# Kernel optimization log

Measured on AMD Instinct MI355X. Metric: run time of the kernel, lower is better.

The kernel has to match this reference:

```python
import jax, jax.numpy as jnp
import numpy as np

B, S, E, HD = 8, 2048, 1024, 64  # batch, seq, n_embds, head_size (n_embds // n_heads)


def setup_inputs() -> dict:
    key = jax.random.key(0)
    k1, k2, k3, k4 = jax.random.split(key, 4)
    x = jax.random.normal(k1, (B, S, E), dtype=jnp.float32)
    # torch Linear weights have shape [out_features, in_features]; scale like default init
    Wk = jax.random.normal(k2, (HD, E), dtype=jnp.float32) * (1.0 / np.sqrt(E))
    Wq = jax.random.normal(k3, (HD, E), dtype=jnp.float32) * (1.0 / np.sqrt(E))
    Wv = jax.random.normal(k4, (HD, E), dtype=jnp.float32) * (1.0 / np.sqrt(E))
    return {"x": x, "Wk": Wk, "Wq": Wq, "Wv": Wv}


def reference(x, Wk, Wq, Wv):
    # q, k, v: [B, S, HD]
    k = jnp.einsum('bse,he->bsh', x, Wk)
    q = jnp.einsum('bse,he->bsh', x, Wq)
    v = jnp.einsum('bse,he->bsh', x, Wv)
    # scores: [B, S, S], scaled by sqrt(head_size)
    scores = jnp.einsum('bqh,bkh->bqk', q, k) / jnp.sqrt(jnp.float32(HD))
    # causal mask (tril): position q attends to k <= q
    causal = jnp.tril(jnp.ones((S, S), dtype=bool))
    scores = jnp.where(causal, scores, jnp.float32(-jnp.inf))
    attn = jax.nn.softmax(scores, axis=-1)
    # dropout_rate = 0.0 -> identity
    out = jnp.einsum('bqk,bkh->bqh', attn, v)  # [B, S, HD]
    return out
```

## Files before the change

### kernel.cpp

```cpp
#include <hip/hip_runtime.h>
#include <hip/hip_bf16.h>
#include <stdint.h>

typedef short bh8 __attribute__((ext_vector_type(8)));
typedef short bh4 __attribute__((ext_vector_type(4)));
typedef float fx4 __attribute__((ext_vector_type(4)));

#define B_ 8
#define S_ 2048
#define E_ 1024
#define HD_ 64

__device__ __forceinline__ short f2bf(float f) {
  unsigned u = __builtin_bit_cast(unsigned, f);
  u = u + 0x7FFFu + ((u >> 16) & 1u);
  return (short)(u >> 16);
}

#define GL2LDS16(gp, lp) __builtin_amdgcn_global_load_lds( \
    (const __attribute__((address_space(1))) unsigned int*)(gp), \
    (__attribute__((address_space(3))) unsigned int*)(lp), 16, 0, 0)


__global__ __launch_bounds__(256) void castw_k(
    const float* __restrict__ wk, const float* __restrict__ wq,
    const float* __restrict__ wv, short* __restrict__ wc) {
  int i = blockIdx.x * 256 + threadIdx.x;
  int wsel = i >> 13;
  int o = (i & 8191) * 8;
  const float* src = (wsel == 0) ? wk : (wsel == 1) ? wq : wv;
  float4 a = *(const float4*)(src + o);
  float4 b = *(const float4*)(src + o + 4);
  bh8 r = { f2bf(a.x), f2bf(a.y), f2bf(a.z), f2bf(a.w),
            f2bf(b.x), f2bf(b.y), f2bf(b.z), f2bf(b.w) };
  *(bh8*)(wc + wsel * (HD_ * E_) + o) = r;
}

__global__ __launch_bounds__(256) void qkv_gemm(
    const float* __restrict__ x, const short* __restrict__ wc,
    short* __restrict__ kfr, short* __restrict__ qfr, short* __restrict__ vfr) {
  __shared__ short As[32 * 32];
  __shared__ short Bs[192 * 32];
  const int tid = threadIdx.x;
  const int w = tid >> 6, l = tid & 63;
  const int c = l & 15, g = l >> 4;
  const int r0 = blockIdx.x * 32;
  const int srow = l >> 2;
  const int scol = (l & 3) * 8;
  const int ar = tid >> 3;
  const int ac = (tid & 7) * 4;

  fx4 acc[2][3];
#pragma unroll
  for (int rt = 0; rt < 2; ++rt)
#pragma unroll
    for (int cc = 0; cc < 3; ++cc) acc[rt][cc] = (fx4){0.f, 0.f, 0.f, 0.f};

  for (int k0 = 0; k0 < E_; k0 += 32) {
    float4 av = *(const float4*)(x + (size_t)(r0 + ar) * E_ + k0 + ac);
    __syncthreads();
#pragma unroll
    for (int p = 0; p < 3; ++p)
      GL2LDS16(wc + (size_t)(16 * (w + 4 * p) + srow) * E_ + k0 + scol,
               &Bs[(w + 4 * p) * 512]);
    bh4 aw = { f2bf(av.x), f2bf(av.y), f2bf(av.z), f2bf(av.w) };
    *(bh4*)&As[ar * 32 + ac] = aw;
    __syncthreads();

    bh8 af[2], bf[3];
    af[0] = *(const bh8*)&As[c * 32 + 8 * g];
    af[1] = *(const bh8*)&As[(16 + c) * 32 + 8 * g];
#pragma unroll
    for (int cc = 0; cc < 3; ++cc)
      bf[cc] = *(const bh8*)&Bs[(16 * (3 * w + cc) + c) * 32 + 8 * g];
#pragma unroll
    for (int rt = 0; rt < 2; ++rt)
#pragma unroll
      for (int cc = 0; cc < 3; ++cc)
        acc[rt][cc] = __builtin_amdgcn_mfma_f32_16x16x32_bf16(af[rt], bf[cc], acc[rt][cc], 0, 0, 0);
  }

#pragma unroll
  for (int rt = 0; rt < 2; ++rt) {
    const int rbase = r0 + 16 * rt + 4 * g;
    const int bb = rbase >> 11;
    const int srw = rbase & (S_ - 1);
    const int kt = srw >> 4;
    const int g2 = (srw & 15) >> 2;
#pragma unroll
    for (int cc = 0; cc < 3; ++cc) {
      const int ctg = 3 * w + cc;
      const int n = 16 * ctg + c;
      if (ctg < 4) {
        const int h = n >> 5, gg = (n & 31) >> 3, jj = n & 7;
        short* dst = kfr + ((size_t)(((bb * 128 + kt) * 2 + h) * 64 + gg * 16) * 8) + jj;
#pragma unroll
        for (int j = 0; j < 4; ++j)
          dst[(size_t)(((rbase + j) & 15)) * 8] = f2bf(acc[rt][cc][j]);
      } else if (ctg < 8) {
        const int nq = n - 64;
        const int h = nq >> 5, gg = (nq & 31) >> 3, jj = nq & 7;
        short* dst = qfr + ((size_t)(((bb * 128 + kt) * 2 + h) * 64 + gg * 16) * 8) + jj;
#pragma unroll
        for (int j = 0; j < 4; ++j)
          dst[(size_t)(((rbase + j) & 15)) * 8] = f2bf(acc[rt][cc][j] * 0.125f);
      } else {
        const int hd = n - 128;
        const int mm = hd >> 4, c2 = hd & 15;
        bh4 pk = { f2bf(acc[rt][cc][0]), f2bf(acc[rt][cc][1]),
                   f2bf(acc[rt][cc][2]), f2bf(acc[rt][cc][3]) };
        *(bh4*)&vfr[(size_t)(((bb * 128 + kt) * 4 + mm) * 64 + g2 * 16 + c2) * 4] = pk;
      }
    }
  }
}

__global__ __launch_bounds__(512) void attn_fused2(
    const short* __restrict__ qfr, const short* __restrict__ kfr,
    const short* __restrict__ vfr, float* __restrict__ out) {
  __shared__ float sO[8][16][68];
  __shared__ float sL[8][16];
  const int tid = threadIdx.x;
  const int w = tid >> 6, l = tid & 63;
  const int c = l & 15, g = l >> 4;
  const int b = blockIdx.x >> 6, p = blockIdx.x & 63;

  const short* qbB = qfr + (size_t)(b * 128) * 1024;
  const short* kbB = kfr + (size_t)(b * 128) * 1024;
  const short* vbB = vfr + (size_t)(b * 128) * 1024;

  for (int qsel = 0; qsel < 2; ++qsel) {
    const int qt = qsel ? (127 - p) : p;
    const int nt = qt + 1;
    const int cnt = (nt + 7) >> 3;
    const int start = w * cnt;
    const int end = min(start + cnt, nt);

    fx4 o[4];
    o[0] = o[1] = o[2] = o[3] = (fx4){0.f, 0.f, 0.f, 0.f};
    float lsum = 0.f;

    if (start < end) {
      bh8 qf0 = *(const bh8*)(qbB + (qt * 2 + 0) * 512 + l * 8);
      bh8 qf1 = *(const bh8*)(qbB + (qt * 2 + 1) * 512 + l * 8);
#pragma unroll 4
      for (int kt = start; kt < end; ++kt) {
        const short* kp = kbB + kt * 1024;
        bh8 kf0 = *(const bh8*)(kp + l * 8);
        bh8 kf1 = *(const bh8*)(kp + 512 + l * 8);
        const short* vp = vbB + kt * 1024;
        bh4 vf0 = *(const bh4*)(vp + l * 4);
        bh4 vf1 = *(const bh4*)(vp + 256 + l * 4);
        bh4 vf2 = *(const bh4*)(vp + 512 + l * 4);
        bh4 vf3 = *(const bh4*)(vp + 768 + l * 4);

        fx4 s = {0.f, 0.f, 0.f, 0.f};
        s = __builtin_amdgcn_mfma_f32_16x16x32_bf16(kf0, qf0, s, 0, 0, 0);
        s = __builtin_amdgcn_mfma_f32_16x16x32_bf16(kf1, qf1, s, 0, 0, 0);
        if (kt == qt) {
#pragma unroll
          for (int j = 0; j < 4; ++j)
            if (4 * g + j > c) s[j] = -1e30f;
        }
        const float p0 = __expf(s[0] - 8.f);
        const float p1 = __expf(s[1] - 8.f);
        const float p2 = __expf(s[2] - 8.f);
        const float p3 = __expf(s[3] - 8.f);
        lsum += (p0 + p1) + (p2 + p3);
        bh4 pf = { f2bf(p0), f2bf(p1), f2bf(p2), f2bf(p3) };
        o[0] = __builtin_amdgcn_mfma_f32_16x16x16bf16_1k(vf0, pf, o[0], 0, 0, 0);
        o[1] = __builtin_amdgcn_mfma_f32_16x16x16bf16_1k(vf1, pf, o[1], 0, 0, 0);
        o[2] = __builtin_amdgcn_mfma_f32_16x16x16bf16_1k(vf2, pf, o[2], 0, 0, 0);
        o[3] = __builtin_amdgcn_mfma_f32_16x16x16bf16_1k(vf3, pf, o[3], 0, 0, 0);
      }
    }

#pragma unroll
    for (int mm = 0; mm < 4; ++mm)
      *(fx4*)&sO[w][c][16 * mm + 4 * g] = o[mm];
    lsum += __shfl_xor(lsum, 16, 64);
    lsum += __shfl_xor(lsum, 32, 64);
    if (g == 0) sL[w][c] = lsum;
    __syncthreads();

    if (w < 4) {
      const int r = tid >> 4;
      const int cg4 = (tid & 15) * 4;
      fx4 a = {0.f, 0.f, 0.f, 0.f};
      float L = 0.f;
#pragma unroll
      for (int i = 0; i < 8; ++i) {
        a += *(const fx4*)&sO[i][r][cg4];
        L += sL[i][r];
      }
      const float inv = 1.0f / L;
      fx4 res = a * inv;
      *(fx4*)(out + ((size_t)(b * S_ + qt * 16 + r)) * HD_ + cg4) = res;
    }
    __syncthreads();
  }
}

extern "C" void kernel_launch(void* const* d_in, const int* in_sizes, int n_in,
                              void* d_out, int out_size, void* d_ws, size_t ws_size,
                              hipStream_t stream) {
  const float* x  = (const float*)d_in[0];
  const float* wk = (const float*)d_in[1];
  const float* wq = (const float*)d_in[2];
  const float* wv = (const float*)d_in[3];
  float* out = (float*)d_out;
  char* ws = (char*)d_ws;
  short* wc  = (short*)(ws);
  short* kfr = (short*)(ws + 393216);
  short* qfr = (short*)(ws + 2490368);
  short* vfr = (short*)(ws + 4587520);

  castw_k<<<dim3(96), dim3(256), 0, stream>>>(wk, wq, wv, wc);
  qkv_gemm<<<dim3(512), dim3(256), 0, stream>>>(x, wc, kfr, qfr, vfr);
  attn_fused2<<<dim3(512), dim3(512), 0, stream>>>(qfr, kfr, vfr, out);
}
```

Before: 50.84 us.

## Double-buffer QKV GEMM loads and process both query tiles in one K/V pass

The QKV projection GEMM now double-buffers its A and B tiles in LDS. The next k-slice's global-to-LDS loads and x prefetch are issued before the current MFMAs, with a single waitcnt and barrier per iteration. The attention kernel now handles its paired query tiles (p and 127-p) in one interleaved sweep over key tiles, so each K/V fragment load serves both tiles. This is meant to hide GEMM load latency and halve K/V reloads in attention, at the cost of more registers and LDS. The hand-written waitcnt and scheduling barriers add fragility.

```diff
diff --git a/kernel.cpp b/kernel.cpp
--- a/kernel.cpp
+++ b/kernel.cpp
@@ -39,8 +39,8 @@
 __global__ __launch_bounds__(256) void qkv_gemm(
     const float* __restrict__ x, const short* __restrict__ wc,
     short* __restrict__ kfr, short* __restrict__ qfr, short* __restrict__ vfr) {
-  __shared__ short As[32 * 32];
-  __shared__ short Bs[192 * 32];
+  __shared__ short As[2][32 * 32];
+  __shared__ short Bs[2][192 * 32];
   const int tid = threadIdx.x;
   const int w = tid >> 6, l = tid & 63;
   const int c = l & 15, g = l >> 4;
@@ -49,6 +49,7 @@
   const int scol = (l & 3) * 8;
   const int ar = tid >> 3;
   const int ac = (tid & 7) * 4;
+  const float* xrow = x + (size_t)(r0 + ar) * E_ + ac;
 
   fx4 acc[2][3];
 #pragma unroll
@@ -56,28 +57,54 @@
 #pragma unroll
     for (int cc = 0; cc < 3; ++cc) acc[rt][cc] = (fx4){0.f, 0.f, 0.f, 0.f};
 
-  for (int k0 = 0; k0 < E_; k0 += 32) {
-    float4 av = *(const float4*)(x + (size_t)(r0 + ar) * E_ + k0 + ac);
-    __syncthreads();
+  float4 av = *(const float4*)(xrow);
+  {
+    bh4 aw = { f2bf(av.x), f2bf(av.y), f2bf(av.z), f2bf(av.w) };
+    *(bh4*)&As[0][ar * 32 + ac] = aw;
 #pragma unroll
     for (int p = 0; p < 3; ++p)
-      GL2LDS16(wc + (size_t)(16 * (w + 4 * p) + srow) * E_ + k0 + scol,
-               &Bs[(w + 4 * p) * 512]);
-    bh4 aw = { f2bf(av.x), f2bf(av.y), f2bf(av.z), f2bf(av.w) };
-    *(bh4*)&As[ar * 32 + ac] = aw;
-    __syncthreads();
+      GL2LDS16(wc + (size_t)(16 * (w + 4 * p) + srow) * E_ + scol,
+               &Bs[0][(w + 4 * p) * 512]);
+    av = *(const float4*)(xrow + 32);
+    __builtin_amdgcn_sched_barrier(0);
+    asm volatile("s_waitcnt vmcnt(1) lgkmcnt(0)" ::: "memory");
+    __builtin_amdgcn_s_barrier();
+    __builtin_amdgcn_sched_barrier(0);
+  }
+
+  for (int t = 0; t < 32; ++t) {
+    const int cur = t & 1;
+    if (t < 31) {
+      bh4 aw = { f2bf(av.x), f2bf(av.y), f2bf(av.z), f2bf(av.w) };
+      *(bh4*)&As[cur ^ 1][ar * 32 + ac] = aw;
+      const int k1 = (t + 1) * 32;
+#pragma unroll
+      for (int p = 0; p < 3; ++p)
+        GL2LDS16(wc + (size_t)(16 * (w + 4 * p) + srow) * E_ + k1 + scol,
+                 &Bs[cur ^ 1][(w + 4 * p) * 512]);
+      const int k2 = (t + 2 < 32) ? (t + 2) * 32 : 0;
+      av = *(const float4*)(xrow + k2);
+      __builtin_amdgcn_sched_barrier(0);
+    }
 
     bh8 af[2], bf[3];
-    af[0] = *(const bh8*)&As[c * 32 + 8 * g];
-    af[1] = *(const bh8*)&As[(16 + c) * 32 + 8 * g];
+    af[0] = *(const bh8*)&As[cur][c * 32 + 8 * g];
+    af[1] = *(const bh8*)&As[cur][(16 + c) * 32 + 8 * g];
 #pragma unroll
     for (int cc = 0; cc < 3; ++cc)
-      bf[cc] = *(const bh8*)&Bs[(16 * (3 * w + cc) + c) * 32 + 8 * g];
+      bf[cc] = *(const bh8*)&Bs[cur][(16 * (3 * w + cc) + c) * 32 + 8 * g];
 #pragma unroll
     for (int rt = 0; rt < 2; ++rt)
 #pragma unroll
       for (int cc = 0; cc < 3; ++cc)
         acc[rt][cc] = __builtin_amdgcn_mfma_f32_16x16x32_bf16(af[rt], bf[cc], acc[rt][cc], 0, 0, 0);
+
+    if (t < 31) {
+      __builtin_amdgcn_sched_barrier(0);
+      asm volatile("s_waitcnt vmcnt(1) lgkmcnt(0)" ::: "memory");
+      __builtin_amdgcn_s_barrier();
+      __builtin_amdgcn_sched_barrier(0);
+    }
   }
 
 #pragma unroll
@@ -115,7 +142,7 @@
   }
 }
 
-__global__ __launch_bounds__(512) void attn_fused2(
+__global__ __launch_bounds__(512, 4) void attn_fused3(
     const short* __restrict__ qfr, const short* __restrict__ kfr,
     const short* __restrict__ vfr, float* __restrict__ out) {
   __shared__ float sO[8][16][68];
@@ -124,80 +151,107 @@
   const int w = tid >> 6, l = tid & 63;
   const int c = l & 15, g = l >> 4;
   const int b = blockIdx.x >> 6, p = blockIdx.x & 63;
+  const int qtA = p, qtB = 127 - p;
 
   const short* qbB = qfr + (size_t)(b * 128) * 1024;
   const short* kbB = kfr + (size_t)(b * 128) * 1024;
   const short* vbB = vfr + (size_t)(b * 128) * 1024;
 
-  for (int qsel = 0; qsel < 2; ++qsel) {
-    const int qt = qsel ? (127 - p) : p;
-    const int nt = qt + 1;
-    const int cnt = (nt + 7) >> 3;
-    const int start = w * cnt;
-    const int end = min(start + cnt, nt);
-
-    fx4 o[4];
-    o[0] = o[1] = o[2] = o[3] = (fx4){0.f, 0.f, 0.f, 0.f};
-    float lsum = 0.f;
-
-    if (start < end) {
-      bh8 qf0 = *(const bh8*)(qbB + (qt * 2 + 0) * 512 + l * 8);
-      bh8 qf1 = *(const bh8*)(qbB + (qt * 2 + 1) * 512 + l * 8);
-#pragma unroll 4
-      for (int kt = start; kt < end; ++kt) {
-        const short* kp = kbB + kt * 1024;
-        bh8 kf0 = *(const bh8*)(kp + l * 8);
-        bh8 kf1 = *(const bh8*)(kp + 512 + l * 8);
-        const short* vp = vbB + kt * 1024;
-        bh4 vf0 = *(const bh4*)(vp + l * 4);
-        bh4 vf1 = *(const bh4*)(vp + 256 + l * 4);
-        bh4 vf2 = *(const bh4*)(vp + 512 + l * 4);
-        bh4 vf3 = *(const bh4*)(vp + 768 + l * 4);
-
-        fx4 s = {0.f, 0.f, 0.f, 0.f};
-        s = __builtin_amdgcn_mfma_f32_16x16x32_bf16(kf0, qf0, s, 0, 0, 0);
-        s = __builtin_amdgcn_mfma_f32_16x16x32_bf16(kf1, qf1, s, 0, 0, 0);
-        if (kt == qt) {
-#pragma unroll
-          for (int j = 0; j < 4; ++j)
-            if (4 * g + j > c) s[j] = -1e30f;
-        }
-        const float p0 = __expf(s[0] - 8.f);
-        const float p1 = __expf(s[1] - 8.f);
-        const float p2 = __expf(s[2] - 8.f);
-        const float p3 = __expf(s[3] - 8.f);
-        lsum += (p0 + p1) + (p2 + p3);
-        bh4 pf = { f2bf(p0), f2bf(p1), f2bf(p2), f2bf(p3) };
-        o[0] = __builtin_amdgcn_mfma_f32_16x16x16bf16_1k(vf0, pf, o[0], 0, 0, 0);
-        o[1] = __builtin_amdgcn_mfma_f32_16x16x16bf16_1k(vf1, pf, o[1], 0, 0, 0);
-        o[2] = __builtin_amdgcn_mfma_f32_16x16x16bf16_1k(vf2, pf, o[2], 0, 0, 0);
-        o[3] = __builtin_amdgcn_mfma_f32_16x16x16bf16_1k(vf3, pf, o[3], 0, 0, 0);
+  bh8 qA0 = *(const bh8*)(qbB + (qtA * 2 + 0) * 512 + l * 8);
+  bh8 qA1 = *(const bh8*)(qbB + (qtA * 2 + 1) * 512 + l * 8);
+  bh8 qB0 = *(const bh8*)(qbB + (qtB * 2 + 0) * 512 + l * 8);
+  bh8 qB1 = *(const bh8*)(qbB + (qtB * 2 + 1) * 512 + l * 8);
+
+  fx4 oA[4], oB[4];
+#pragma unroll
+  for (int mm = 0; mm < 4; ++mm) { oA[mm] = (fx4){0,0,0,0}; oB[mm] = (fx4){0,0,0,0}; }
+  float lA = 0.f, lB = 0.f;
+
+  for (int kt = w; kt <= qtB; kt += 8) {
+    const short* kp = kbB + kt * 1024;
+    bh8 kf0 = *(const bh8*)(kp + l * 8);
+    bh8 kf1 = *(const bh8*)(kp + 512 + l * 8);
+    const short* vp = vbB + kt * 1024;
+    bh4 vf0 = *(const bh4*)(vp + l * 4);
+    bh4 vf1 = *(const bh4*)(vp + 256 + l * 4);
+    bh4 vf2 = *(const bh4*)(vp + 512 + l * 4);
+    bh4 vf3 = *(const bh4*)(vp + 768 + l * 4);
+
+    fx4 sB = {0.f, 0.f, 0.f, 0.f};
+    sB = __builtin_amdgcn_mfma_f32_16x16x32_bf16(kf0, qB0, sB, 0, 0, 0);
+    sB = __builtin_amdgcn_mfma_f32_16x16x32_bf16(kf1, qB1, sB, 0, 0, 0);
+    if (kt == qtB) {
+#pragma unroll
+      for (int j = 0; j < 4; ++j)
+        if (4 * g + j > c) sB[j] = -1e30f;
+    }
+    const float pB0 = __expf(sB[0] - 8.f);
+    const float pB1 = __expf(sB[1] - 8.f);
+    const float pB2 = __expf(sB[2] - 8.f);
+    const float pB3 = __expf(sB[3] - 8.f);
+    lB += (pB0 + pB1) + (pB2 + pB3);
+    bh4 pfB = { f2bf(pB0), f2bf(pB1), f2bf(pB2), f2bf(pB3) };
+    oB[0] = __builtin_amdgcn_mfma_f32_16x16x16bf16_1k(vf0, pfB, oB[0], 0, 0, 0);
+    oB[1] = __builtin_amdgcn_mfma_f32_16x16x16bf16_1k(vf1, pfB, oB[1], 0, 0, 0);
+    oB[2] = __builtin_amdgcn_mfma_f32_16x16x16bf16_1k(vf2, pfB, oB[2], 0, 0, 0);
+    oB[3] = __builtin_amdgcn_mfma_f32_16x16x16bf16_1k(vf3, pfB, oB[3], 0, 0, 0);
+
+    if (kt <= qtA) {
+      fx4 sA = {0.f, 0.f, 0.f, 0.f};
+      sA = __builtin_amdgcn_mfma_f32_16x16x32_bf16(kf0, qA0, sA, 0, 0, 0);
+      sA = __builtin_amdgcn_mfma_f32_16x16x32_bf16(kf1, qA1, sA, 0, 0, 0);
+      if (kt == qtA) {
+#pragma unroll
+        for (int j = 0; j < 4; ++j)
+          if (4 * g + j > c) sA[j] = -1e30f;
       }
-    }
-
-#pragma unroll
-    for (int mm = 0; mm < 4; ++mm)
-      *(fx4*)&sO[w][c][16 * mm + 4 * g] = o[mm];
-    lsum += __shfl_xor(lsum, 16, 64);
-    lsum += __shfl_xor(lsum, 32, 64);
-    if (g == 0) sL[w][c] = lsum;
-    __syncthreads();
-
-    if (w < 4) {
-      const int r = tid >> 4;
-      const int cg4 = (tid & 15) * 4;
-      fx4 a = {0.f, 0.f, 0.f, 0.f};
-      float L = 0.f;
-#pragma unroll
-      for (int i = 0; i < 8; ++i) {
-        a += *(const fx4*)&sO[i][r][cg4];
-        L += sL[i][r];
-      }
-      const float inv = 1.0f / L;
-      fx4 res = a * inv;
-      *(fx4*)(out + ((size_t)(b * S_ + qt * 16 + r)) * HD_ + cg4) = res;
-    }
-    __syncthreads();
+      const float pA0 = __expf(sA[0] - 8.f);
+      const float pA1 = __expf(sA[1] - 8.f);
+      const float pA2 = __expf(sA[2] - 8.f);
+      const float pA3 = __expf(sA[3] - 8.f);
+      lA += (pA0 + pA1) + (pA2 + pA3);
+      bh4 pfA = { f2bf(pA0), f2bf(pA1), f2bf(pA2), f2bf(pA3) };
+      oA[0] = __builtin_amdgcn_mfma_f32_16x16x16bf16_1k(vf0, pfA, oA[0], 0, 0, 0);
+      oA[1] = __builtin_amdgcn_mfma_f32_16x16x16bf16_1k(vf1, pfA, oA[1], 0, 0, 0);
+      oA[2] = __builtin_amdgcn_mfma_f32_16x16x16bf16_1k(vf2, pfA, oA[2], 0, 0, 0);
+      oA[3] = __builtin_amdgcn_mfma_f32_16x16x16bf16_1k(vf3, pfA, oA[3], 0, 0, 0);
+    }
+  }
+
+#pragma unroll
+  for (int mm = 0; mm < 4; ++mm)
+    *(fx4*)&sO[w][c][16 * mm + 4 * g] = oA[mm];
+  lA += __shfl_xor(lA, 16, 64);
+  lA += __shfl_xor(lA, 32, 64);
+  if (g == 0) sL[w][c] = lA;
+  __syncthreads();
+  if (w < 4) {
+    const int r = tid >> 4;
+    const int cg4 = (tid & 15) * 4;
+    fx4 a = {0.f, 0.f, 0.f, 0.f};
+    float L = 0.f;
+#pragma unroll
+    for (int i = 0; i < 8; ++i) { a += *(const fx4*)&sO[i][r][cg4]; L += sL[i][r]; }
+    fx4 res = a * (1.0f / L);
+    *(fx4*)(out + ((size_t)(b * S_ + qtA * 16 + r)) * HD_ + cg4) = res;
+  }
+  __syncthreads();
+#pragma unroll
+  for (int mm = 0; mm < 4; ++mm)
+    *(fx4*)&sO[w][c][16 * mm + 4 * g] = oB[mm];
+  lB += __shfl_xor(lB, 16, 64);
+  lB += __shfl_xor(lB, 32, 64);
+  if (g == 0) sL[w][c] = lB;
+  __syncthreads();
+  if (w < 4) {
+    const int r = tid >> 4;
+    const int cg4 = (tid & 15) * 4;
+    fx4 a = {0.f, 0.f, 0.f, 0.f};
+    float L = 0.f;
+#pragma unroll
+    for (int i = 0; i < 8; ++i) { a += *(const fx4*)&sO[i][r][cg4]; L += sL[i][r]; }
+    fx4 res = a * (1.0f / L);
+    *(fx4*)(out + ((size_t)(b * S_ + qtB * 16 + r)) * HD_ + cg4) = res;
   }
 }
 
@@ -217,5 +271,5 @@
 
   castw_k<<<dim3(96), dim3(256), 0, stream>>>(wk, wq, wv, wc);
   qkv_gemm<<<dim3(512), dim3(256), 0, stream>>>(x, wc, kfr, qfr, vfr);
-  attn_fused2<<<dim3(512), dim3(512), 0, stream>>>(qfr, kfr, vfr, out);
-}
+  attn_fused3<<<dim3(512), dim3(512), 0, stream>>>(qfr, kfr, vfr, out);
+}
```

Result: faster. 49.67 us (-2.3%).
